# Performance work log

Hardware: AMD Instinct MI355X
Metric: run time of the kernel (lower is better)

Reference implementation:

```python
import jax, jax.numpy as jnp
import numpy as np

T, B, H, K = 512, 64, 512, 16  # seq_len, batch, hidden_size, num_tags


def setup_inputs() -> dict:
    key = jax.random.key(0)
    ks = jax.random.split(key, 8)
    hidden = jax.random.normal(ks[0], (T, B, H), dtype=jnp.float32)
    W1 = jax.random.normal(ks[1], (H, H), dtype=jnp.float32) / np.float32(np.sqrt(H))
    b1 = jnp.zeros((H,), jnp.float32)
    W2 = jax.random.normal(ks[2], (H, K), dtype=jnp.float32) / np.float32(np.sqrt(H))
    b2 = jnp.zeros((K,), jnp.float32)
    transition = jax.random.normal(ks[3], (K, K), dtype=jnp.float32)
    lens = jax.random.randint(ks[4], (B,), T // 2, T + 1)  # valid lengths in [T/2, T]
    tags = jax.random.randint(ks[5], (T, B), 0, K)
    return dict(hidden=hidden, W1=W1, b1=b1, W2=W2, b2=b2,
                transition=transition, lens=lens, tags=tags)


def reference(hidden, W1, b1, W2, b2, transition, lens, tags):
    # Emission MLP (dropout is identity in eval): Linear -> ReLU -> Linear
    h = jax.nn.relu(hidden @ W1 + b1)          # [T, B, H]
    em = h @ W2 + b2                           # [T, B, K]

    # ---- forward (partition) score: linear-chain logsumexp DP ----
    def step(alpha, e_t):
        # alpha: [B, K] over prev tags; transition[curr, prev]
        a = jax.nn.logsumexp(alpha[:, None, :] + transition[None, :, :], axis=-1) + e_t
        return a, a

    alpha0 = em[0]
    _, alphas = jax.lax.scan(step, alpha0, em[1:])
    alphas = jnp.concatenate([alpha0[None], alphas], axis=0)            # [T, B, K]
    last = jnp.take_along_axis(alphas, (lens - 1)[None, :, None], axis=0)[0]  # [B, K]
    fwd_score = jax.nn.logsumexp(last, axis=-1)                          # [B]

    # ---- gold path score ----
    em_path = jnp.take_along_axis(em, tags[:, :, None], axis=-1)[..., 0]  # [T, B]
    trans_path = transition[tags[1:], tags[:-1]]                          # [T-1, B]
    steps = em_path.at[1:].add(trans_path)
    cum = jnp.cumsum(steps, axis=0)                                       # [T, B]
    gold = jnp.take_along_axis(cum, (lens - 1)[None, :], axis=0)[0]       # [B]

    return (fwd_score - gold).sum()
```

## Files before the change

### kernel.cpp

```cpp
#include <hip/hip_runtime.h>
#include <hip/hip_bf16.h>

#define TT 512
#define BB 64
#define HH 512
#define KK 16

#define NCH 32
#define CST (TT / NCH)

typedef __attribute__((ext_vector_type(8))) short bf16x8;
typedef __attribute__((ext_vector_type(4))) short bf16x4;
typedef __attribute__((ext_vector_type(4))) float f32x4;

#define MFMA_K16(A, B, C) __builtin_amdgcn_mfma_f32_16x16x16bf16_1k(A, B, C, 0, 0, 0)

__device__ __forceinline__ unsigned short f2bf(float f) {
    union { __hip_bfloat16 h; unsigned short u; } cvt;
    cvt.h = __float2bfloat16(f);
    return cvt.u;
}

__device__ __forceinline__ short rne_bf(float x) {
    unsigned u = __float_as_uint(x);
    u += 0x7fffu + ((u >> 16) & 1u);
    return (short)(u >> 16);
}

__device__ __forceinline__ float bf2f(short s) {
    return __uint_as_float(((unsigned)(unsigned short)s) << 16);
}

__global__ void prep_kernel(const float* __restrict__ W1, const float* __restrict__ W2,
                            unsigned short* __restrict__ W1t, unsigned short* __restrict__ W2t,
                            float* __restrict__ out) {
    const int bi = blockIdx.x, tx = threadIdx.x;
    if (bi < 64) {
        __shared__ float Ls[64][65];
        const int ti = bi & 7, tj = bi >> 3;
        const int r0 = ti * 64, c0 = tj * 64;
        const int r = tx >> 4, c4 = (tx & 15) * 4;
#pragma unroll
        for (int i = 0; i < 4; ++i) {
            float4 v = *(const float4*)(W1 + (size_t)(r0 + r + 16 * i) * HH + c0 + c4);
            Ls[c4 + 0][r + 16 * i] = v.x;
            Ls[c4 + 1][r + 16 * i] = v.y;
            Ls[c4 + 2][r + 16 * i] = v.z;
            Ls[c4 + 3][r + 16 * i] = v.w;
        }
        __syncthreads();
        const int rn = tx >> 4, k4 = (tx & 15) * 4;
#pragma unroll
        for (int i = 0; i < 4; ++i) {
            const int n = rn + 16 * i;
            ushort4 o;
            o.x = f2bf(Ls[n][k4 + 0]);
            o.y = f2bf(Ls[n][k4 + 1]);
            o.z = f2bf(Ls[n][k4 + 2]);
            o.w = f2bf(Ls[n][k4 + 3]);
            *(ushort4*)(W1t + (size_t)(c0 + n) * HH + r0 + k4) = o;
        }
    } else {
        if (tx == 0) out[0] = 0.0f;
        for (int idx = tx; idx < 16 * HH; idx += 256) {
            const int n = idx >> 9, k = idx & 511;
            W2t[idx] = f2bf(W2[k * KK + n]);
        }
    }
}

__global__ __launch_bounds__(256, 2)
void em_kernel(const float* __restrict__ hidden, const unsigned short* __restrict__ W1t,
               const float* __restrict__ b1, const unsigned short* __restrict__ W2t,
               const float* __restrict__ b2, float* __restrict__ em) {
    __shared__ unsigned short W2ts[16 * 520];
    __shared__ __align__(16) unsigned char stage[37888];
    unsigned short* As = (unsigned short*)stage;
    unsigned short* Bs = (unsigned short*)(stage + 5120);
    unsigned short* Hb = (unsigned short*)stage;

    const int tx = threadIdx.x;
    const int w = tx >> 6, lane = tx & 63;
    const int q = lane >> 4, nl = lane & 15;
    const int wm = w >> 1, wn = w & 1;
    const int row0 = blockIdx.x * 64;

    for (int i = tx; i < 16 * 64; i += 256) {
        const int n = i >> 6, kc = i & 63;
        *(bf16x8*)(W2ts + n * 520 + kc * 8) = *(const bf16x8*)(W2t + n * HH + kc * 8);
    }

    f32x4 acc[2][16];
#pragma unroll
    for (int mt = 0; mt < 2; ++mt)
#pragma unroll
        for (int nt = 0; nt < 16; ++nt) acc[mt][nt] = (f32x4){0.f, 0.f, 0.f, 0.f};

    for (int kt = 0; kt < 16; ++kt) {
        const int k0 = kt * 32;
        __syncthreads();
        {
            const int r = tx >> 2, c8 = (tx & 3) * 8;
            const float* src = hidden + (size_t)(row0 + r) * HH + k0 + c8;
            float4 v0 = *(const float4*)(src);
            float4 v1 = *(const float4*)(src + 4);
            bf16x8 o;
            o[0] = (short)f2bf(v0.x); o[1] = (short)f2bf(v0.y);
            o[2] = (short)f2bf(v0.z); o[3] = (short)f2bf(v0.w);
            o[4] = (short)f2bf(v1.x); o[5] = (short)f2bf(v1.y);
            o[6] = (short)f2bf(v1.z); o[7] = (short)f2bf(v1.w);
            *(bf16x8*)(As + r * 40 + c8) = o;
        }
#pragma unroll
        for (int it = 0; it < 8; ++it) {
            const int c = it * 256 + tx;
            const int n = c >> 2, slot = c & 3;
            const int kc = slot ^ ((n >> 1) & 3);
            __builtin_amdgcn_global_load_lds(
                (const __attribute__((address_space(1))) void*)(W1t + (size_t)n * HH + k0 + kc * 8),
                (__attribute__((address_space(3))) void*)(Bs + c * 8),
                16, 0, 0);
        }
        __syncthreads();
        bf16x8 af[2];
#pragma unroll
        for (int mt = 0; mt < 2; ++mt)
            af[mt] = *(const bf16x8*)(As + (32 * wm + 16 * mt + nl) * 40 + q * 8);
#pragma unroll
        for (int nt = 0; nt < 16; ++nt) {
            const int n = 256 * wn + 16 * nt + nl;
            const int slot = q ^ ((n >> 1) & 3);
            bf16x8 bf = *(const bf16x8*)(Bs + n * 32 + slot * 8);
            acc[0][nt] = __builtin_amdgcn_mfma_f32_16x16x32_bf16(af[0], bf, acc[0][nt], 0, 0, 0);
            acc[1][nt] = __builtin_amdgcn_mfma_f32_16x16x32_bf16(af[1], bf, acc[1][nt], 0, 0, 0);
        }
    }

    f32x4 acc2 = (f32x4){0.f, 0.f, 0.f, 0.f};
    for (int c = 0; c < 2; ++c) {
        __syncthreads();
        if (wn == c) {
#pragma unroll
            for (int nt = 0; nt < 16; ++nt) {
                const float bv = b1[c * 256 + 16 * nt + nl];
#pragma unroll
                for (int mt = 0; mt < 2; ++mt) {
#pragma unroll
                    for (int r = 0; r < 4; ++r) {
                        float v = acc[mt][nt][r] + bv;
                        v = v > 0.f ? v : 0.f;
                        const int row = 32 * wm + 16 * mt + q * 4 + r;
                        Hb[row * 264 + nt * 16 + nl] = f2bf(v);
                    }
                }
            }
        }
        __syncthreads();
#pragma unroll
        for (int ks = 0; ks < 8; ++ks) {
            bf16x8 a2 = *(const bf16x8*)(Hb + (16 * w + nl) * 264 + ks * 32 + q * 8);
            bf16x8 b2f = *(const bf16x8*)(W2ts + nl * 520 + c * 256 + ks * 32 + q * 8);
            acc2 = __builtin_amdgcn_mfma_f32_16x16x32_bf16(a2, b2f, acc2, 0, 0, 0);
        }
    }
#pragma unroll
    for (int r = 0; r < 4; ++r) {
        const int row = row0 + 16 * w + q * 4 + r;
        em[(size_t)row * KK + nl] = acc2[r] + b2[nl];
    }
}

__global__ void scan_gold_kernel(const float* __restrict__ em, const float* __restrict__ trans,
                                 const int* __restrict__ lens, const int* __restrict__ tags,
                                 float* __restrict__ Pfull, float* __restrict__ Cfull,
                                 float* __restrict__ Ppart, float* __restrict__ Cpart,
                                 float* __restrict__ out) {
    __shared__ float trs[256];
    __shared__ float red[4];
    const int tx = threadIdx.x;

    if (blockIdx.x >= 512) {
        trs[tx] = __logf(bf2f(rne_bf(__expf(trans[tx]))));
        __syncthreads();
        const int idx = (blockIdx.x - 512) * 256 + tx;
        const int t = idx >> 6, b = idx & 63;
        const int L = lens[b];
        float v = 0.0f;
        if (t < L) {
            const int tg = tags[t * BB + b];
            v = em[((size_t)t * BB + b) * KK + tg];
            if (t > 0) v += trs[tg * 16 + tags[(t - 1) * BB + b]];
        }
#pragma unroll
        for (int dd = 1; dd < 64; dd <<= 1) v += __shfl_xor(v, dd, 64);
        if ((tx & 63) == 0) red[tx >> 6] = v;
        __syncthreads();
        if (tx == 0) atomicAdd(out, -(red[0] + red[1] + red[2] + red[3]));
        return;
    }

    const int id = blockIdx.x * 4 + (tx >> 6);
    const int lane = tx & 63, q = lane >> 4, col = lane & 15;
    const int b = id >> 5, c = id & 31;

    float mf[4];
    {
        float4 tv = *(const float4*)(trans + col * 16 + 4 * q);
        mf[0] = bf2f(rne_bf(__expf(tv.x)));
        mf[1] = bf2f(rne_bf(__expf(tv.y)));
        mf[2] = bf2f(rne_bf(__expf(tv.z)));
        mf[3] = bf2f(rne_bf(__expf(tv.w)));
    }
    const int Lm1 = lens[b] - 1;
    const int tb0 = CST * c;

    float ebuf[8];
#pragma unroll
    for (int i = 0; i < 8; ++i)
        ebuf[i] = em[(size_t)((tb0 + i) * BB + b) * KK + col];

    bf16x4 gb;
#pragma unroll
    for (int i = 0; i < 4; ++i)
        gb[i] = (4 * q + i == col) ? rne_bf(1.0f) : (short)0;

    const f32x4 zc = (f32x4){0.f, 0.f, 0.f, 0.f};
    f32x4 d = (f32x4){0.f, 0.f, 0.f, 0.f};
    float K = 1.0f, rk = 1.0f, lk = 0.0f, Cacc = 0.0f;

    for (int sb = 0; sb < CST; sb += 8) {
        const bool refill = (sb < CST - 8);
#pragma unroll
        for (int s8 = 0; s8 < 8; ++s8) {
            const int t = tb0 + sb + s8;
            const float eraw = ebuf[s8];
            if (refill)
                ebuf[s8] = em[(size_t)((t + 8) * BB + b) * KK + col];
            float ev = __expf(eraw);
            if ((s8 & 3) == 0 && (sb + s8) >= 4) {
                ev *= rk;
                Cacc += lk;
            }
            bf16x4 af;
            af[0] = rne_bf(ev * mf[0]); af[1] = rne_bf(ev * mf[1]);
            af[2] = rne_bf(ev * mf[2]); af[3] = rne_bf(ev * mf[3]);
            if (s8 == 0) {
                if (sb == 0 && c == 0) {
#pragma unroll
                    for (int i = 0; i < 4; ++i)
                        af[i] = (4 * q + i == col) ? rne_bf(ev) : (short)0;
                }
            }
            d = MFMA_K16(af, gb, zc);
            if ((s8 & 3) == 1) {
                K = __shfl(d[0], 0, 64);
                const float Km = fmaxf(K, 1e-30f);
                rk = 1.0f / Km;
                lk = __logf(Km);
            }
            if (t == Lm1) {
#pragma unroll
                for (int r = 0; r < 4; ++r)
                    Ppart[b * 256 + (4 * q + r) * 16 + col] = d[r];
                if (lane == 0) Cpart[b] = Cacc;
            }
            gb[0] = rne_bf(d[0]); gb[1] = rne_bf(d[1]);
            gb[2] = rne_bf(d[2]); gb[3] = rne_bf(d[3]);
        }
    }
#pragma unroll
    for (int r = 0; r < 4; ++r)
        Pfull[(size_t)(b * NCH + c) * 256 + (4 * q + r) * 16 + col] = d[r];
    if (lane == 0) Cfull[b * NCH + c] = Cacc;
}

__global__ void combine_kernel(const int* __restrict__ lens,
                               const float* __restrict__ Pfull, const float* __restrict__ Cfull,
                               const float* __restrict__ Ppart, const float* __restrict__ Cpart,
                               float* __restrict__ out) {
    const int lane = threadIdx.x;
    const int grp = lane >> 4, j = lane & 15;
    const int b = blockIdx.x * 4 + grp;
    const int base = grp << 4;
    const int cstar = (lens[b] - 1) / CST;

    float g = 1.0f, acc = 0.0f;
    for (int c = 0; c < NCH; ++c) {
        const bool act = (c <= cstar);
        const float* P = (c < cstar) ? (Pfull + (size_t)(b * NCH + c) * 256)
                                     : (Ppart + b * 256);
        float gn = 0.0f;
#pragma unroll
        for (int k = 0; k < 16; ++k) {
            const float gk = __shfl(g, base + k, 64);
            gn += P[j * 16 + k] * gk;
        }
        if (act) {
            float m = gn;
#pragma unroll
            for (int dd = 1; dd < 16; dd <<= 1) m = fmaxf(m, __shfl_xor(m, dd, 64));
            g = gn / m;
            acc += __logf(m) + ((c < cstar) ? Cfull[b * NCH + c] : Cpart[b]);
        }
    }
    float ssum = g;
#pragma unroll
    for (int dd = 1; dd < 16; dd <<= 1) ssum += __shfl_xor(ssum, dd, 64);
    const float fwd = acc + __logf(ssum);
    if (j == 0) atomicAdd(out, fwd);
}

extern "C" void kernel_launch(void* const* d_in, const int* in_sizes, int n_in,
                              void* d_out, int out_size, void* d_ws, size_t ws_size,
                              hipStream_t stream) {
    const float* hidden = (const float*)d_in[0];
    const float* W1     = (const float*)d_in[1];
    const float* b1     = (const float*)d_in[2];
    const float* W2     = (const float*)d_in[3];
    const float* b2     = (const float*)d_in[4];
    const float* trans  = (const float*)d_in[5];
    const int*   lens   = (const int*)d_in[6];
    const int*   tags   = (const int*)d_in[7];
    float* out = (float*)d_out;

    char* ws = (char*)d_ws;
    float* em = (float*)ws;
    unsigned short* W1t = (unsigned short*)(ws + 2097152);
    unsigned short* W2t = (unsigned short*)(ws + 2621440);
    float* Pfull = (float*)(ws + 2637824);
    float* Cfull = (float*)(ws + 4734976);
    float* Ppart = (float*)(ws + 4743168);
    float* Cpart = (float*)(ws + 4808704);

    prep_kernel<<<65, 256, 0, stream>>>(W1, W2, W1t, W2t, out);
    em_kernel<<<512, 256, 0, stream>>>(hidden, W1t, b1, W2t, b2, em);
    scan_gold_kernel<<<640, 256, 0, stream>>>(em, trans, lens, tags,
                                              Pfull, Cfull, Ppart, Cpart, out);
    combine_kernel<<<16, 64, 0, stream>>>(lens, Pfull, Cfull, Ppart, Cpart, out);
}
```

Baseline: 160.0 us.

## Halve scan chunk count and fuse combine into scan via last-block arrival counter

Reduces the number of scan chunks per sequence from 32 to 16, so each wave runs a longer serial chain but there are fewer chunk matrices to combine. The separate combine kernel is removed: each scan block bumps a per-batch atomic counter, and the last of the four blocks for a batch element performs the chunk-matrix combination and accumulates the forward score. This removes one kernel launch and shortens the serial combine loop, at the cost of longer per-chunk scans and threadfence/atomic synchronisation.

```diff
diff --git a/kernel.cpp b/kernel.cpp
--- a/kernel.cpp
+++ b/kernel.cpp
@@ -6,7 +6,7 @@
 #define HH 512
 #define KK 16
 
-#define NCH 32
+#define NCH 16
 #define CST (TT / NCH)
 
 typedef __attribute__((ext_vector_type(8))) short bf16x8;
@@ -33,7 +33,7 @@
 
 __global__ void prep_kernel(const float* __restrict__ W1, const float* __restrict__ W2,
                             unsigned short* __restrict__ W1t, unsigned short* __restrict__ W2t,
-                            float* __restrict__ out) {
+                            int* __restrict__ cnt, float* __restrict__ out) {
     const int bi = blockIdx.x, tx = threadIdx.x;
     if (bi < 64) {
         __shared__ float Ls[64][65];
@@ -62,6 +62,7 @@
         }
     } else {
         if (tx == 0) out[0] = 0.0f;
+        if (tx < 64) cnt[tx] = 0;
         for (int idx = tx; idx < 16 * HH; idx += 256) {
             const int n = idx >> 9, k = idx & 511;
             W2t[idx] = f2bf(W2[k * KK + n]);
@@ -174,15 +175,16 @@
                                  const int* __restrict__ lens, const int* __restrict__ tags,
                                  float* __restrict__ Pfull, float* __restrict__ Cfull,
                                  float* __restrict__ Ppart, float* __restrict__ Cpart,
-                                 float* __restrict__ out) {
+                                 int* __restrict__ cnt, float* __restrict__ out) {
     __shared__ float trs[256];
     __shared__ float red[4];
+    __shared__ int arrival;
     const int tx = threadIdx.x;
 
-    if (blockIdx.x >= 512) {
+    if (blockIdx.x >= 256) {
         trs[tx] = __logf(bf2f(rne_bf(__expf(trans[tx]))));
         __syncthreads();
-        const int idx = (blockIdx.x - 512) * 256 + tx;
+        const int idx = (blockIdx.x - 256) * 256 + tx;
         const int t = idx >> 6, b = idx & 63;
         const int L = lens[b];
         float v = 0.0f;
@@ -201,7 +203,7 @@
 
     const int id = blockIdx.x * 4 + (tx >> 6);
     const int lane = tx & 63, q = lane >> 4, col = lane & 15;
-    const int b = id >> 5, c = id & 31;
+    const int b = id >> 4, c = id & 15;
 
     float mf[4];
     {
@@ -272,23 +274,24 @@
     for (int r = 0; r < 4; ++r)
         Pfull[(size_t)(b * NCH + c) * 256 + (4 * q + r) * 16 + col] = d[r];
     if (lane == 0) Cfull[b * NCH + c] = Cacc;
-}
-
-__global__ void combine_kernel(const int* __restrict__ lens,
-                               const float* __restrict__ Pfull, const float* __restrict__ Cfull,
-                               const float* __restrict__ Ppart, const float* __restrict__ Cpart,
-                               float* __restrict__ out) {
-    const int lane = threadIdx.x;
-    const int grp = lane >> 4, j = lane & 15;
-    const int b = blockIdx.x * 4 + grp;
+
+    __threadfence();
+    __syncthreads();
+    if (tx == 0) arrival = atomicAdd(&cnt[b], 1);
+    __syncthreads();
+    if (arrival != 3) return;
+    __threadfence();
+    if (tx >= 64) return;
+
+    const int grp = tx >> 4, j = tx & 15;
     const int base = grp << 4;
     const int cstar = (lens[b] - 1) / CST;
 
     float g = 1.0f, acc = 0.0f;
-    for (int c = 0; c < NCH; ++c) {
-        const bool act = (c <= cstar);
-        const float* P = (c < cstar) ? (Pfull + (size_t)(b * NCH + c) * 256)
-                                     : (Ppart + b * 256);
+    for (int cc = 0; cc < NCH; ++cc) {
+        const bool act = (cc <= cstar);
+        const float* P = (cc < cstar) ? (Pfull + (size_t)(b * NCH + cc) * 256)
+                                      : (Ppart + b * 256);
         float gn = 0.0f;
 #pragma unroll
         for (int k = 0; k < 16; ++k) {
@@ -300,14 +303,14 @@
 #pragma unroll
             for (int dd = 1; dd < 16; dd <<= 1) m = fmaxf(m, __shfl_xor(m, dd, 64));
             g = gn / m;
-            acc += __logf(m) + ((c < cstar) ? Cfull[b * NCH + c] : Cpart[b]);
+            acc += __logf(m) + ((cc < cstar) ? Cfull[b * NCH + cc] : Cpart[b]);
         }
     }
     float ssum = g;
 #pragma unroll
     for (int dd = 1; dd < 16; dd <<= 1) ssum += __shfl_xor(ssum, dd, 64);
     const float fwd = acc + __logf(ssum);
-    if (j == 0) atomicAdd(out, fwd);
+    if (tx == 0) atomicAdd(out, fwd);
 }
 
 extern "C" void kernel_launch(void* const* d_in, const int* in_sizes, int n_in,
@@ -328,13 +331,13 @@
     unsigned short* W1t = (unsigned short*)(ws + 2097152);
     unsigned short* W2t = (unsigned short*)(ws + 2621440);
     float* Pfull = (float*)(ws + 2637824);
-    float* Cfull = (float*)(ws + 4734976);
-    float* Ppart = (float*)(ws + 4743168);
-    float* Cpart = (float*)(ws + 4808704);
-
-    prep_kernel<<<65, 256, 0, stream>>>(W1, W2, W1t, W2t, out);
+    float* Cfull = (float*)(ws + 3686400);
+    float* Ppart = (float*)(ws + 3690496);
+    float* Cpart = (float*)(ws + 3756032);
+    int*   cnt   = (int*)(ws + 3756288);
+
+    prep_kernel<<<65, 256, 0, stream>>>(W1, W2, W1t, W2t, cnt, out);
     em_kernel<<<512, 256, 0, stream>>>(hidden, W1t, b1, W2t, b2, em);
-    scan_gold_kernel<<<640, 256, 0, stream>>>(em, trans, lens, tags,
-                                              Pfull, Cfull, Ppart, Cpart, out);
-    combine_kernel<<<16, 64, 0, stream>>>(lens, Pfull, Cfull, Ppart, Cpart, out);
-}
+    scan_gold_kernel<<<384, 256, 0, stream>>>(em, trans, lens, tags,
+                                              Pfull, Cfull, Ppart, Cpart, cnt, out);
+}
```

Result: slower. 180.1 us (+12.6%).
